# Kernel tuning notes

Hardware: AMD Instinct MI355X
Metric: run time of the kernel (lower is better)

## Reference

```python
import jax, jax.numpy as jnp
import numpy as np

D_MODEL = 1024
NUM_HEADS = 16
D_K = D_MODEL // NUM_HEADS


def setup_inputs() -> dict:
    key = jax.random.key(0)
    ks = jax.random.split(key, 9)
    s = 1.0 / np.sqrt(D_MODEL)
    inp = {
        "x": jax.random.normal(ks[0], (4, 2048, D_MODEL), dtype=jnp.float32),
        "W_q": jax.random.uniform(ks[1], (D_MODEL, D_MODEL), jnp.float32, -s, s),
        "b_q": jax.random.uniform(ks[2], (D_MODEL,), jnp.float32, -s, s),
        "W_k": jax.random.uniform(ks[3], (D_MODEL, D_MODEL), jnp.float32, -s, s),
        "b_k": jax.random.uniform(ks[4], (D_MODEL,), jnp.float32, -s, s),
        "W_v": jax.random.uniform(ks[5], (D_MODEL, D_MODEL), jnp.float32, -s, s),
        "b_v": jax.random.uniform(ks[6], (D_MODEL,), jnp.float32, -s, s),
        "W_o": jax.random.uniform(ks[7], (D_MODEL, D_MODEL), jnp.float32, -s, s),
        "b_o": jax.random.uniform(ks[8], (D_MODEL,), jnp.float32, -s, s),
    }
    return inp


def reference(x, W_q, b_q, W_k, b_k, W_v, b_v, W_o, b_o):
    B, S, _ = x.shape
    # Linear layers (torch convention: y = x @ W.T + b), split into heads -> [B, H, S, d_k]
    def proj(W, b):
        y = jnp.einsum("bsd,ed->bse", x, W) + b
        return y.reshape(B, S, NUM_HEADS, D_K).transpose(0, 2, 1, 3)

    Q = proj(W_q, b_q)
    K = proj(W_k, b_k)
    V = proj(W_v, b_v)

    scale = 1.0 / jnp.sqrt(jnp.asarray(D_K, dtype=x.dtype))
    scores = jnp.einsum("bhqd,bhkd->bhqk", Q, K) * scale  # [B, H, S, S]
    attn = jax.nn.softmax(scores, axis=-1)
    out = jnp.einsum("bhqk,bhkd->bhqd", attn, V)  # [B, H, S, d_k]
    out = out.transpose(0, 2, 1, 3).reshape(B, S, D_MODEL)
    return jnp.einsum("bsd,ed->bse", out, W_o) + b_o
```

## Files before the change

### kernel.cpp

```cpp
#include <hip/hip_runtime.h>
#include <hip/hip_bf16.h>
#include <math.h>


constexpr int D = 1024;
constexpr int H = 16;
constexpr int DK = 64;
constexpr int PSTR = 72;

typedef unsigned short u16;
typedef __attribute__((ext_vector_type(8))) short v8s;
typedef __attribute__((ext_vector_type(4))) float v4f;
typedef const __attribute__((address_space(1))) void gvoid;
typedef __attribute__((address_space(3))) void lvoid;
typedef __attribute__((address_space(3))) u16 ls_u16;
typedef __attribute__((address_space(3))) v8s lv8s;

__device__ __forceinline__ u16 rne_bf16(float f) {
  unsigned u = __float_as_uint(f);
  u += 0x7FFFu + ((u >> 16) & 1u);
  return (u16)(u >> 16);
}

__device__ __forceinline__ unsigned pk_bf16(float a, float b) {
  __hip_bfloat162 t = __float22bfloat162_rn(float2{a, b});
  return *reinterpret_cast<unsigned*>(&t);
}

__device__ __forceinline__ void cfence() { asm volatile("" ::: "memory"); }

__device__ __forceinline__ void split_body(const float* __restrict__ in,
                                           u16* __restrict__ hi, u16* __restrict__ lo,
                                           int i)
{
  const float4 v = ((const float4*)in)[i];
  const float f[4] = {v.x, v.y, v.z, v.w};
  ushort4 h, l;
  u16 hh[4], ll[4];
#pragma unroll
  for (int j = 0; j < 4; ++j) {
    const unsigned u = __float_as_uint(f[j]);
    hh[j] = (u16)(u >> 16);
    const float hf = __uint_as_float(u & 0xFFFF0000u);
    ll[j] = rne_bf16(f[j] - hf);
  }
  h.x = hh[0]; h.y = hh[1]; h.z = hh[2]; h.w = hh[3];
  l.x = ll[0]; l.y = ll[1]; l.z = ll[2]; l.w = ll[3];
  ((ushort4*)hi)[i] = h;
  ((ushort4*)lo)[i] = l;
}

__global__ __launch_bounds__(256) void split_kernel(
    const float* __restrict__ in, u16* __restrict__ hi, u16* __restrict__ lo, int n4)
{
  const int i = blockIdx.x * 256 + threadIdx.x;
  if (i >= n4) return;
  split_body(in, hi, lo, i);
}

__global__ __launch_bounds__(256) void splitw_kernel(
    const float* __restrict__ w0, const float* __restrict__ w1,
    const float* __restrict__ w2, const float* __restrict__ w3,
    u16* __restrict__ qkv_hi, u16* __restrict__ qkv_lo,
    u16* __restrict__ o_hi, u16* __restrict__ o_lo, int n4)
{
  const int i = blockIdx.x * 256 + threadIdx.x;
  if (i >= n4) return;
  const int y = blockIdx.y;
  const float* src = (y == 0) ? w0 : (y == 1) ? w1 : (y == 2) ? w2 : w3;
  const size_t off = (size_t)y * (size_t)n4;
  u16* hi = (y < 3) ? qkv_hi + off * 4 : o_hi;
  u16* lo = (y < 3) ? qkv_lo + off * 4 : o_lo;
  split_body(src, hi, lo, i);
}

template<int R>
__device__ __forceinline__ void stage_arr(const u16* __restrict__ src, ls_u16* dst,
                                          int tid, int row0, int k0)
{
  const int cg = (tid & 3) ^ ((tid >> 3) & 3);
#pragma unroll
  for (int j = 0; j < R / 128; ++j) {
    const int row = j * 128 + (tid >> 2);
    __builtin_amdgcn_global_load_lds(
        (gvoid*)(src + (size_t)(row0 + row) * D + k0 + cg * 8),
        (lvoid*)(dst + j * 4096 + tid * 8), 16, 0, 0);
  }
}

template<int BM, int BN, int EPI>
__global__ __launch_bounds__(512, 2) void gemm_pipe_kernel(
    const u16* __restrict__ Ahi, const u16* __restrict__ Alo,
    const u16* __restrict__ Whi, const u16* __restrict__ Wlo,
    const float* __restrict__ b0v, const float* __restrict__ b1v, const float* __restrict__ b2v,
    u16* __restrict__ Qb, u16* __restrict__ Kb, u16* __restrict__ Vtb,
    float* __restrict__ C, int S_)
{
  constexpr int TA = BM * 32;
  constexpr int TB = BN * 32;
  constexpr int BUFSZ = 2 * TA + 2 * TB;
  __shared__ u16 lds[3][BUFSZ];

  const int tid = threadIdx.x;
  const int lane = tid & 63, w = tid >> 6;
  const int wm = (w >> 1) * 64, wn = (w & 1) * 64;
  const int fr = lane & 15, fq = lane >> 4;
  const int csw = (fq ^ ((fr >> 1) & 3)) * 8;

  const int gx = gridDim.x;
  const int gyd = gridDim.y;
  const int nwg = gx * gyd;
  int id = blockIdx.y * gx + blockIdx.x;
  id = (id & 7) * (nwg >> 3) + (id >> 3);
  constexpr int GM = 4;
  const int per_grp = GM * gyd;
  const int grp = id / per_grp;
  const int ing = id - grp * per_grp;
  const int m0 = (grp * GM + (ing & (GM - 1))) * BM;
  const int n0 = (ing / GM) * BN;

  v4f acc[4][4];
#pragma unroll
  for (int mi = 0; mi < 4; ++mi)
#pragma unroll
    for (int ni = 0; ni < 4; ++ni) acc[mi][ni] = (v4f){0.f, 0.f, 0.f, 0.f};

  ls_u16* pb0 = (ls_u16*)&lds[0][0];
  ls_u16* pb1 = (ls_u16*)&lds[1][0];
  ls_u16* pb2 = (ls_u16*)&lds[2][0];

  int aoff[4], boff[4];
#pragma unroll
  for (int i = 0; i < 4; ++i) {
    aoff[i] = (wm + i * 16 + fr) * 32 + csw;
    boff[i] = 2 * TA + (wn + i * 16 + fr) * 32 + csw;
  }

#pragma unroll
  for (int p = 0; p < 2; ++p) {
    ls_u16* pb = (p == 0) ? pb0 : pb1;
    stage_arr<BM>(Ahi, pb, tid, m0, p * 32);
    stage_arr<BM>(Alo, pb + TA, tid, m0, p * 32);
    stage_arr<BN>(Whi, pb + 2 * TA, tid, n0, p * 32);
    stage_arr<BN>(Wlo, pb + 2 * TA + TB, tid, n0, p * 32);
  }

#pragma unroll 2
  for (int k = 0; k < 32; ++k) {
    const int ks = (k + 2 < 32) ? (k + 2) * 32 : 31 * 32;

    asm volatile("s_waitcnt vmcnt(6)" ::: "memory");
    __builtin_amdgcn_s_barrier();
    cfence();

    v8s ah[4], bh[4], tf[4];
#pragma unroll
    for (int i = 0; i < 4; ++i) ah[i] = *(const lv8s*)(pb0 + aoff[i]);
#pragma unroll
    for (int i = 0; i < 4; ++i) bh[i] = *(const lv8s*)(pb0 + boff[i]);
    stage_arr<BM>(Ahi, pb2, tid, m0, ks);
    __builtin_amdgcn_s_setprio(1);
#pragma unroll
    for (int mi = 0; mi < 4; ++mi)
#pragma unroll
      for (int ni = 0; ni < 4; ++ni)
        acc[mi][ni] = __builtin_amdgcn_mfma_f32_16x16x32_bf16(ah[mi], bh[ni], acc[mi][ni], 0, 0, 0);
    __builtin_amdgcn_s_setprio(0);
    cfence();
    __builtin_amdgcn_s_barrier();
    cfence();

#pragma unroll
    for (int i = 0; i < 4; ++i) tf[i] = *(const lv8s*)(pb0 + TA + aoff[i]);
    stage_arr<BM>(Alo, pb2 + TA, tid, m0, ks);
    __builtin_amdgcn_s_setprio(1);
#pragma unroll
    for (int mi = 0; mi < 4; ++mi)
#pragma unroll
      for (int ni = 0; ni < 4; ++ni)
        acc[mi][ni] = __builtin_amdgcn_mfma_f32_16x16x32_bf16(tf[mi], bh[ni], acc[mi][ni], 0, 0, 0);
    __builtin_amdgcn_s_setprio(0);
    cfence();
    __builtin_amdgcn_s_barrier();
    cfence();

#pragma unroll
    for (int i = 0; i < 4; ++i) tf[i] = *(const lv8s*)(pb0 + boff[i] + TB);
    stage_arr<BN>(Whi, pb2 + 2 * TA, tid, n0, ks);
    stage_arr<BN>(Wlo, pb2 + 2 * TA + TB, tid, n0, ks);
    __builtin_amdgcn_s_setprio(1);
#pragma unroll
    for (int mi = 0; mi < 4; ++mi)
#pragma unroll
      for (int ni = 0; ni < 4; ++ni)
        acc[mi][ni] = __builtin_amdgcn_mfma_f32_16x16x32_bf16(ah[mi], tf[ni], acc[mi][ni], 0, 0, 0);
    __builtin_amdgcn_s_setprio(0);
    cfence();

    ls_u16* t = pb0; pb0 = pb1; pb1 = pb2; pb2 = t;
  }

  const int lane4 = fq * 4;
  if constexpr (EPI == 0) {
    const int wsel = n0 >> 10;
    const float* bias = (wsel == 0) ? b0v : (wsel == 1) ? b1v : b2v;
    u16* Cb = (wsel == 0) ? Qb : (wsel == 1) ? Kb : Vtb;
    const int bb = m0 / S_;
    const int s0 = m0 - bb * S_;
#pragma unroll
    for (int mi = 0; mi < 4; ++mi) {
#pragma unroll
      for (int ni = 0; ni < 4; ++ni) {
        const int n = n0 + wn + ni * 16 + fr;
        const int nl = n & (D - 1);
        const float bvv = bias[nl];
        const int h = nl >> 6, dk = nl & 63;
#pragma unroll
        for (int r = 0; r < 4; ++r) {
          const int s = s0 + wm + mi * 16 + lane4 + r;
          const float val = acc[mi][ni][r] + bvv;
          if (wsel < 2)
            Cb[((size_t)(bb * H + h) * S_ + s) * DK + dk] = rne_bf16(val);
          else
            Cb[((size_t)(bb * H + h) * DK + dk) * S_ + s] = rne_bf16(val);
        }
      }
    }
  } else {
#pragma unroll
    for (int mi = 0; mi < 4; ++mi)
#pragma unroll
      for (int ni = 0; ni < 4; ++ni) {
        const int n = n0 + wn + ni * 16 + fr;
        const float bvv = b0v[n];
#pragma unroll
        for (int r = 0; r < 4; ++r) {
          const int m = m0 + wm + mi * 16 + lane4 + r;
          C[(size_t)m * D + n] = acc[mi][ni][r] + bvv;
        }
      }
  }
}

__global__ __launch_bounds__(256) void attn_mfma_kernel(
    const u16* __restrict__ Qb, const u16* __restrict__ Kb, const u16* __restrict__ Vtb,
    u16* __restrict__ Ohi, u16* __restrict__ Olo, int S_)
{
  __shared__ u16 Ks[2][64 * 64];
  __shared__ u16 Vt[2][64 * 64];
  __shared__ u16 Pl[4][32 * PSTR];

  const int tid = threadIdx.x;
  const int lane = tid & 63, w = tid >> 6;
  const int fr = lane & 15, fq = lane >> 4;
  const int q0 = blockIdx.x * 128;
  const int h = blockIdx.y, b = blockIdx.z;
  const int wq = w * 32;
  const size_t base = (size_t)(b * H + h) * S_ * DK;

  const int srow = tid >> 3;
  const int scb = (tid & 7) ^ (srow & 7);

  auto stage_kv = [&](int j0, int bufi) {
#pragma unroll
    for (int rep = 0; rep < 2; ++rep) {
      const int row = rep * 32 + srow;
      const int ldso = rep * 2048 + tid * 8;
      __builtin_amdgcn_global_load_lds((gvoid*)(Kb + base + (size_t)(j0 + row) * DK + scb * 8),
                                       (lvoid*)(&Ks[bufi][0] + ldso), 16, 0, 0);
      __builtin_amdgcn_global_load_lds((gvoid*)(Vtb + base + (size_t)row * S_ + j0 + scb * 8),
                                       (lvoid*)(&Vt[bufi][0] + ldso), 16, 0, 0);
    }
  };

  stage_kv(0, 0);

  v8s qa[2][2];
#pragma unroll
  for (int ni = 0; ni < 2; ++ni)
#pragma unroll
    for (int ks = 0; ks < 2; ++ks)
      qa[ni][ks] = *(const v8s*)(Qb + base + (size_t)(q0 + wq + ni * 16 + fr) * DK + ks * 32 + fq * 8);

  v4f o[4][2];
  float lsum[2] = {0.f, 0.f};
#pragma unroll
  for (int mi = 0; mi < 4; ++mi)
#pragma unroll
    for (int ni = 0; ni < 2; ++ni) o[mi][ni] = (v4f){0.f, 0.f, 0.f, 0.f};

  asm volatile("s_waitcnt vmcnt(0)" ::: "memory");
  __builtin_amdgcn_s_barrier();
  cfence();

  const int NT = S_ >> 6;
  for (int jt = 0; jt < NT; ++jt) {
    const int cur = jt & 1;
    if (jt + 1 < NT) stage_kv((jt + 1) * 64, cur ^ 1);

    const u16* Kc = &Ks[cur][0];
    const u16* Vc = &Vt[cur][0];

    v4f s[4][2];
#pragma unroll
    for (int mi = 0; mi < 4; ++mi)
#pragma unroll
      for (int ni = 0; ni < 2; ++ni) s[mi][ni] = (v4f){0.f, 0.f, 0.f, 0.f};
#pragma unroll
    for (int ks = 0; ks < 2; ++ks) {
      v8s kb[4];
#pragma unroll
      for (int mi = 0; mi < 4; ++mi) {
        const int row = mi * 16 + fr;
        kb[mi] = *(const v8s*)&Kc[row * 64 + (((ks * 4 + fq) ^ (row & 7)) * 8)];
      }
#pragma unroll
      for (int mi = 0; mi < 4; ++mi)
#pragma unroll
        for (int ni = 0; ni < 2; ++ni)
          s[mi][ni] = __builtin_amdgcn_mfma_f32_16x16x32_bf16(kb[mi], qa[ni][ks], s[mi][ni], 0, 0, 0);
    }

#pragma unroll
    for (int mi = 0; mi < 4; ++mi)
#pragma unroll
      for (int ni = 0; ni < 2; ++ni) {
        float p[4];
#pragma unroll
        for (int r = 0; r < 4; ++r) p[r] = __expf(s[mi][ni][r] * 0.125f);
        lsum[ni] += (p[0] + p[1]) + (p[2] + p[3]);
        uint2 pk;
        pk.x = pk_bf16(p[0], p[1]);
        pk.y = pk_bf16(p[2], p[3]);
        *(uint2*)&Pl[w][(ni * 16 + fr) * PSTR + mi * 16 + fq * 4] = pk;
      }

#pragma unroll
    for (int ks = 0; ks < 2; ++ks) {
      v8s vb[4], pa[2];
#pragma unroll
      for (int mi = 0; mi < 4; ++mi) {
        const int row = mi * 16 + fr;
        vb[mi] = *(const v8s*)&Vc[row * 64 + (((ks * 4 + fq) ^ (row & 7)) * 8)];
      }
#pragma unroll
      for (int ni = 0; ni < 2; ++ni)
        pa[ni] = *(const v8s*)&Pl[w][(ni * 16 + fr) * PSTR + ks * 32 + fq * 8];
#pragma unroll
      for (int mi = 0; mi < 4; ++mi)
#pragma unroll
        for (int ni = 0; ni < 2; ++ni)
          o[mi][ni] = __builtin_amdgcn_mfma_f32_16x16x32_bf16(vb[mi], pa[ni], o[mi][ni], 0, 0, 0);
    }

    asm volatile("s_waitcnt vmcnt(0)" ::: "memory");
    cfence();
    __builtin_amdgcn_s_barrier();
    cfence();
  }

  float linv[2];
#pragma unroll
  for (int ni = 0; ni < 2; ++ni) {
    float l = lsum[ni];
    l += __shfl_xor(l, 16);
    l += __shfl_xor(l, 32);
    linv[ni] = 1.f / l;
  }

#pragma unroll
  for (int ni = 0; ni < 2; ++ni) {
    const int q = q0 + wq + ni * 16 + fr;
    const size_t rowbase = (size_t)(b * S_ + q) * D + h * DK;
#pragma unroll
    for (int mi = 0; mi < 4; ++mi) {
      const int d0 = mi * 16 + fq * 4;
      float v[4];
      unsigned u[4];
      float res[4];
#pragma unroll
      for (int r = 0; r < 4; ++r) {
        v[r] = o[mi][ni][r] * linv[ni];
        u[r] = __float_as_uint(v[r]);
        res[r] = v[r] - __uint_as_float(u[r] & 0xFFFF0000u);
      }
      uint2 hi, lo;
      hi.x = (u[1] & 0xFFFF0000u) | (u[0] >> 16);
      hi.y = (u[3] & 0xFFFF0000u) | (u[2] >> 16);
      lo.x = pk_bf16(res[0], res[1]);
      lo.y = pk_bf16(res[2], res[3]);
      *(uint2*)(Ohi + rowbase + d0) = hi;
      *(uint2*)(Olo + rowbase + d0) = lo;
    }
  }
}

extern "C" void kernel_launch(void* const* d_in, const int* in_sizes, int n_in,
                              void* d_out, int out_size, void* d_ws, size_t ws_size,
                              hipStream_t stream) {
  const float* x  = (const float*)d_in[0];
  const float* Wq = (const float*)d_in[1];
  const float* bq = (const float*)d_in[2];
  const float* Wk = (const float*)d_in[3];
  const float* bk = (const float*)d_in[4];
  const float* Wv = (const float*)d_in[5];
  const float* bv = (const float*)d_in[6];
  const float* Wo = (const float*)d_in[7];
  const float* bo = (const float*)d_in[8];

  const int M = in_sizes[0] / D;
  const int B = 4;
  const int S_ = M / B;
  const size_t MD = (size_t)M * D;
  const size_t DD = (size_t)D * D;

  u16* Qb    = (u16*)d_ws;
  u16* Kb    = Qb + MD;
  u16* Vtb   = Kb + MD;
  u16* xs_hi = Vtb + MD;
  u16* xs_lo = xs_hi + MD;
  u16* Ohi   = xs_lo + MD;
  u16* Olo   = Ohi + MD;
  u16* wo_hi = Olo + MD;
  u16* wo_lo = wo_hi + DD;

  u16* wqkv_hi = (u16*)d_out;
  u16* wqkv_lo = wqkv_hi + 3 * DD;

  const int gx = (int)(MD / 4 / 256);
  const int gw = (int)(DD / 4 / 256);

  split_kernel<<<gx, 256, 0, stream>>>(x, xs_hi, xs_lo, (int)(MD / 4));
  dim3 gws(gw, 4);
  splitw_kernel<<<gws, 256, 0, stream>>>(Wq, Wk, Wv, Wo, wqkv_hi, wqkv_lo,
                                         wo_hi, wo_lo, (int)(DD / 4));

  dim3 gq(M / 256, 3 * D / 128);
  gemm_pipe_kernel<256, 128, 0><<<gq, 512, 0, stream>>>(
      xs_hi, xs_lo, wqkv_hi, wqkv_lo, bq, bk, bv, Qb, Kb, Vtb, nullptr, S_);

  dim3 ga(S_ / 128, H, B);
  attn_mfma_kernel<<<ga, 256, 0, stream>>>(Qb, Kb, Vtb, Ohi, Olo, S_);

  dim3 go(M / 256, D / 128);
  gemm_pipe_kernel<256, 128, 1><<<go, 512, 0, stream>>>(
      Ohi, Olo, wo_hi, wo_lo, bo, nullptr, nullptr, nullptr, nullptr, nullptr,
      (float*)d_out, S_);
}
```

Baseline: 430.1 us.

## Merge split kernels and enlarge attention blocks to 256 queries with XCD remap

The x and weight split kernels are merged into a single launch to save one kernel launch. The attention kernel now uses 512 threads (8 waves) per block and covers 256 queries, so each K/V tile staged in LDS is shared by twice as many query rows. Block IDs are remapped so that consecutive work lands on the same XCD. This halves global K/V traffic per query but leaves fewer blocks, and the larger shared memory footprint plus the launch-bounds hint may limit occupancy.

```diff
diff --git a/kernel.cpp b/kernel.cpp
--- a/kernel.cpp
+++ b/kernel.cpp
@@ -50,28 +50,29 @@
   ((ushort4*)lo)[i] = l;
 }
 
-__global__ __launch_bounds__(256) void split_kernel(
-    const float* __restrict__ in, u16* __restrict__ hi, u16* __restrict__ lo, int n4)
-{
-  const int i = blockIdx.x * 256 + threadIdx.x;
-  if (i >= n4) return;
-  split_body(in, hi, lo, i);
-}
-
-__global__ __launch_bounds__(256) void splitw_kernel(
+__global__ __launch_bounds__(256) void split_all_kernel(
+    const float* __restrict__ x,
     const float* __restrict__ w0, const float* __restrict__ w1,
     const float* __restrict__ w2, const float* __restrict__ w3,
+    u16* __restrict__ xs_hi, u16* __restrict__ xs_lo,
     u16* __restrict__ qkv_hi, u16* __restrict__ qkv_lo,
-    u16* __restrict__ o_hi, u16* __restrict__ o_lo, int n4)
+    u16* __restrict__ o_hi, u16* __restrict__ o_lo, int n4x)
 {
+  constexpr int N4W = (int)(D * (size_t)D / 4);
   const int i = blockIdx.x * 256 + threadIdx.x;
-  if (i >= n4) return;
-  const int y = blockIdx.y;
+  if (i < n4x) {
+    split_body(x, xs_hi, xs_lo, i);
+    return;
+  }
+  const int t = i - n4x;
+  const int y = t / N4W;
+  const int j = t - y * N4W;
+  if (y >= 4) return;
   const float* src = (y == 0) ? w0 : (y == 1) ? w1 : (y == 2) ? w2 : w3;
-  const size_t off = (size_t)y * (size_t)n4;
-  u16* hi = (y < 3) ? qkv_hi + off * 4 : o_hi;
-  u16* lo = (y < 3) ? qkv_lo + off * 4 : o_lo;
-  split_body(src, hi, lo, i);
+  const size_t off = (size_t)y * (size_t)(D * (size_t)D);
+  u16* hi = (y < 3) ? qkv_hi + off : o_hi;
+  u16* lo = (y < 3) ? qkv_lo + off : o_lo;
+  split_body(src, hi, lo, j);
 }
 
 template<int R>
@@ -242,19 +243,28 @@
   }
 }
 
-__global__ __launch_bounds__(256) void attn_mfma_kernel(
+__global__ __launch_bounds__(512, 4) void attn_mfma_kernel(
     const u16* __restrict__ Qb, const u16* __restrict__ Kb, const u16* __restrict__ Vtb,
     u16* __restrict__ Ohi, u16* __restrict__ Olo, int S_)
 {
   __shared__ u16 Ks[2][64 * 64];
   __shared__ u16 Vt[2][64 * 64];
-  __shared__ u16 Pl[4][32 * PSTR];
+  __shared__ u16 Pl[8][32 * PSTR];
 
   const int tid = threadIdx.x;
   const int lane = tid & 63, w = tid >> 6;
   const int fr = lane & 15, fq = lane >> 4;
-  const int q0 = blockIdx.x * 128;
-  const int h = blockIdx.y, b = blockIdx.z;
+
+  const int gqx = gridDim.x;
+  const int nwg = gqx * gridDim.y * gridDim.z;
+  int id = (blockIdx.z * gridDim.y + blockIdx.y) * gqx + blockIdx.x;
+  id = (id & 7) * (nwg >> 3) + (id >> 3);
+  const int qx = id % gqx;
+  const int rest = id / gqx;
+  const int h = rest % H;
+  const int b = rest / H;
+
+  const int q0 = qx * 256;
   const int wq = w * 32;
   const size_t base = (size_t)(b * H + h) * S_ * DK;
 
@@ -262,15 +272,10 @@
   const int scb = (tid & 7) ^ (srow & 7);
 
   auto stage_kv = [&](int j0, int bufi) {
-#pragma unroll
-    for (int rep = 0; rep < 2; ++rep) {
-      const int row = rep * 32 + srow;
-      const int ldso = rep * 2048 + tid * 8;
-      __builtin_amdgcn_global_load_lds((gvoid*)(Kb + base + (size_t)(j0 + row) * DK + scb * 8),
-                                       (lvoid*)(&Ks[bufi][0] + ldso), 16, 0, 0);
-      __builtin_amdgcn_global_load_lds((gvoid*)(Vtb + base + (size_t)row * S_ + j0 + scb * 8),
-                                       (lvoid*)(&Vt[bufi][0] + ldso), 16, 0, 0);
-    }
+    __builtin_amdgcn_global_load_lds((gvoid*)(Kb + base + (size_t)(j0 + srow) * DK + scb * 8),
+                                     (lvoid*)(&Ks[bufi][0] + tid * 8), 16, 0, 0);
+    __builtin_amdgcn_global_load_lds((gvoid*)(Vtb + base + (size_t)srow * S_ + j0 + scb * 8),
+                                     (lvoid*)(&Vt[bufi][0] + tid * 8), 16, 0, 0);
   };
 
   stage_kv(0, 0);
@@ -427,20 +432,19 @@
   u16* wqkv_hi = (u16*)d_out;
   u16* wqkv_lo = wqkv_hi + 3 * DD;
 
-  const int gx = (int)(MD / 4 / 256);
-  const int gw = (int)(DD / 4 / 256);
-
-  split_kernel<<<gx, 256, 0, stream>>>(x, xs_hi, xs_lo, (int)(MD / 4));
-  dim3 gws(gw, 4);
-  splitw_kernel<<<gws, 256, 0, stream>>>(Wq, Wk, Wv, Wo, wqkv_hi, wqkv_lo,
-                                         wo_hi, wo_lo, (int)(DD / 4));
+  const int n4x = (int)(MD / 4);
+  const int n4w = (int)(DD / 4);
+  const int nsb = (n4x + 4 * n4w + 255) / 256;
+  split_all_kernel<<<nsb, 256, 0, stream>>>(x, Wq, Wk, Wv, Wo,
+                                            xs_hi, xs_lo, wqkv_hi, wqkv_lo,
+                                            wo_hi, wo_lo, n4x);
 
   dim3 gq(M / 256, 3 * D / 128);
   gemm_pipe_kernel<256, 128, 0><<<gq, 512, 0, stream>>>(
       xs_hi, xs_lo, wqkv_hi, wqkv_lo, bq, bk, bv, Qb, Kb, Vtb, nullptr, S_);
 
-  dim3 ga(S_ / 128, H, B);
-  attn_mfma_kernel<<<ga, 256, 0, stream>>>(Qb, Kb, Vtb, Ohi, Olo, S_);
+  dim3 ga(S_ / 256, H, B);
+  attn_mfma_kernel<<<ga, 512, 0, stream>>>(Qb, Kb, Vtb, Ohi, Olo, S_);
 
   dim3 go(M / 256, D / 128);
   gemm_pipe_kernel<256, 128, 1><<<go, 512, 0, stream>>>(
```

New measurement: 394.1 us. 8.4% less time.
